# Kernel tuning notes

Measured on AMD Instinct MI355X. Metric: run time of the kernel, lower is better.

## Reference

```python
import jax, jax.numpy as jnp
import numpy as np

D_SAMPLE = 256
TEMPERATURE = 1.0
BETA = 0.5


def setup_inputs() -> dict:
    key = jax.random.key(0)
    k1, k2, k3, k4 = jax.random.split(key, 4)
    K, D = 64, 1_000_000
    client_tokens = jax.random.normal(k1, (K, D), dtype=jnp.float32)
    global_token = jax.random.normal(k2, (1, D), dtype=jnp.float32)
    # attention_net params: Linear(512,128) -> ReLU -> Linear(128,1)
    W1 = jax.random.normal(k3, (2 * D_SAMPLE, 128), dtype=jnp.float32) * (1.0 / np.sqrt(2 * D_SAMPLE))
    b1 = jnp.zeros((128,), dtype=jnp.float32)
    W2 = jax.random.normal(k4, (128, 1), dtype=jnp.float32) * (1.0 / np.sqrt(128))
    b2 = jnp.zeros((1,), dtype=jnp.float32)
    return {"client_tokens": client_tokens, "global_token": global_token,
            "W1": W1, "b1": b1, "W2": W2, "b2": b2}


def _fixed_size_sample(tokens):
    # gather d_input_sample columns with indices = arange(256) % L
    L = tokens.shape[1]
    idx = jnp.arange(D_SAMPLE, dtype=jnp.int32) % L
    return tokens[:, idx]  # [N, 256]


def reference(client_tokens, global_token, W1, b1, W2, b2):
    K, D = client_tokens.shape
    expanded_global = jnp.broadcast_to(global_token, (K, D))
    client_samples = _fixed_size_sample(client_tokens)      # [K, 256]
    global_samples = _fixed_size_sample(expanded_global)    # [K, 256]
    attn_in = jnp.concatenate([client_samples, global_samples], axis=1).astype(jnp.float32)  # [K, 512]
    h = jax.nn.relu(attn_in @ W1 + b1)                       # [K, 128]
    scores = h @ W2 + b2                                     # [K, 1]
    attention_weights = jax.nn.softmax(scores / TEMPERATURE, axis=0)  # [K, 1]
    fused_by_clients = jnp.sum(client_tokens * attention_weights, axis=0, keepdims=True)  # [1, D]
    fused_token = (1.0 - BETA) * global_token + BETA * fused_by_clients
    return fused_token
```

## Files before the change

kernel.cpp:

```cpp
#include <hip/hip_runtime.h>

#define D_SAMPLE 256
#define KCLIENTS 64
#define NH 128

__global__ void lf_scores_kernel(const float* __restrict__ client,
                                 const float* __restrict__ globalt,
                                 const float* __restrict__ W1,
                                 const float* __restrict__ b1,
                                 const float* __restrict__ W2,
                                 const float* __restrict__ b2,
                                 float* __restrict__ scores,
                                 int D) {
    const int k = blockIdx.x;
    const int t = threadIdx.x;

    __shared__ float attn[2 * D_SAMPLE];
    __shared__ float ph[4][NH];
    __shared__ float red[2];

    if (t < D_SAMPLE)       attn[t] = client[(size_t)k * D + t];
    else                    attn[t] = globalt[t - D_SAMPLE];
    __syncthreads();

    const int q = t >> 7;
    const int j = t & (NH - 1);
    const float* __restrict__ w1p = W1 + (size_t)(q * 128) * NH + j;
    const float* __restrict__ xp  = attn + q * 128;

    float acc = 0.0f;
#pragma unroll 8
    for (int i = 0; i < 128; ++i)
        acc = fmaf(xp[i], w1p[(size_t)i * NH], acc);
    ph[q][j] = acc;
    __syncthreads();

    if (t < NH) {
        float h = b1[j] + ph[0][j] + ph[1][j] + ph[2][j] + ph[3][j];
        h = fmaxf(h, 0.0f);
        float v = h * W2[j];
#pragma unroll
        for (int off = 32; off > 0; off >>= 1)
            v += __shfl_down(v, off, 64);
        if ((t & 63) == 0) red[t >> 6] = v;
    }
    __syncthreads();
    if (t == 0) scores[k] = red[0] + red[1] + b2[0];
}

__global__ void lf_fuse_kernel(const float* __restrict__ client,
                               const float* __restrict__ globalt,
                               const float* __restrict__ scores,
                               float* __restrict__ out,
                               int D4) {
    __shared__ float w[KCLIENTS];
    const int t = threadIdx.x;
    if (t < KCLIENTS) {
        float s = scores[t];
        float m = s;
#pragma unroll
        for (int off = 32; off > 0; off >>= 1)
            m = fmaxf(m, __shfl_xor(m, off, 64));
        float e = __expf(s - m);
        float sum = e;
#pragma unroll
        for (int off = 32; off > 0; off >>= 1)
            sum += __shfl_xor(sum, off, 64);
        w[t] = e / sum;
    }
    __syncthreads();

    const float4* __restrict__ c4 = (const float4*)client;
    const float4* __restrict__ g4 = (const float4*)globalt;
    float4* __restrict__ o4 = (float4*)out;

    int idx = blockIdx.x * blockDim.x + t;
    int stride = gridDim.x * blockDim.x;

    for (int d = idx; d < D4; d += stride) {
        float4 acc = make_float4(0.f, 0.f, 0.f, 0.f);
#pragma unroll 8
        for (int k = 0; k < KCLIENTS; ++k) {
            const float wk = w[k];
            const float4 c = c4[(size_t)k * D4 + d];
            acc.x = fmaf(wk, c.x, acc.x);
            acc.y = fmaf(wk, c.y, acc.y);
            acc.z = fmaf(wk, c.z, acc.z);
            acc.w = fmaf(wk, c.w, acc.w);
        }
        const float4 g = g4[d];
        float4 r;
        r.x = 0.5f * g.x + 0.5f * acc.x;
        r.y = 0.5f * g.y + 0.5f * acc.y;
        r.z = 0.5f * g.z + 0.5f * acc.z;
        r.w = 0.5f * g.w + 0.5f * acc.w;
        o4[d] = r;
    }
}

extern "C" void kernel_launch(void* const* d_in, const int* in_sizes, int n_in,
                              void* d_out, int out_size, void* d_ws, size_t ws_size,
                              hipStream_t stream) {
    const float* client  = (const float*)d_in[0];
    const float* globalt = (const float*)d_in[1];
    const float* W1      = (const float*)d_in[2];
    const float* b1      = (const float*)d_in[3];
    const float* W2      = (const float*)d_in[4];
    const float* b2      = (const float*)d_in[5];
    float* out = (float*)d_out;

    const int D = in_sizes[0] / KCLIENTS;
    const int D4 = D / 4;

    float* scores = (float*)d_ws;

    lf_scores_kernel<<<KCLIENTS, 512, 0, stream>>>(client, globalt, W1, b1, W2, b2,
                                                   scores, D);

    const int block = 256;
    int grid = (D4 + block - 1) / block;
    lf_fuse_kernel<<<grid, block, 0, stream>>>(client, globalt, scores, out, D4);
}
```

Before: 51.33 us.

## Fuse score and fusion kernels via cooperative launch with pre-sync prefetch

Merges the attention-score kernel and the weighted-sum kernel into one cooperative kernel. The first 64 blocks compute the per-client scores, then every block prefetches its first six client rows into shared memory before a grid-wide sync. After the sync, each block computes the softmax and accumulates the remaining rows from global memory. The aim is to remove the second kernel launch and hide the score computation behind useful loads. In exchange it adds a grid-wide barrier and about 24KB of shared memory per block, and it relies on all 977 blocks being co-resident, which the cooperative launch requires but whose return status is not checked.

```diff
diff --git a/kernel.cpp b/kernel.cpp
--- a/kernel.cpp
+++ b/kernel.cpp
@@ -1,60 +1,82 @@
 #include <hip/hip_runtime.h>
+#include <hip/hip_cooperative_groups.h>
+
+namespace cg = cooperative_groups;
 
 #define D_SAMPLE 256
 #define KCLIENTS 64
 #define NH 128
+#define STAGE_K 6
+#define BLOCK 256
 
-__global__ void lf_scores_kernel(const float* __restrict__ client,
-                                 const float* __restrict__ globalt,
-                                 const float* __restrict__ W1,
-                                 const float* __restrict__ b1,
-                                 const float* __restrict__ W2,
-                                 const float* __restrict__ b2,
-                                 float* __restrict__ scores,
-                                 int D) {
-    const int k = blockIdx.x;
+__global__ __launch_bounds__(BLOCK, 4)
+void lf_fused_kernel(const float* __restrict__ client,
+                     const float* __restrict__ globalt,
+                     const float* __restrict__ W1,
+                     const float* __restrict__ b1,
+                     const float* __restrict__ W2,
+                     const float* __restrict__ b2,
+                     float* __restrict__ scores,
+                     float* __restrict__ out,
+                     int D, int D4) {
+    __shared__ float4 stage[STAGE_K][BLOCK];
+    __shared__ float  w[KCLIENTS];
+    __shared__ float  ph[2][NH];
+    __shared__ float  red[2];
+    __shared__ float  attn[2 * D_SAMPLE];
+
     const int t = threadIdx.x;
+    const int b = blockIdx.x;
+    const float4* __restrict__ c4 = (const float4*)client;
+    const float4* __restrict__ g4 = (const float4*)globalt;
+    float4* __restrict__ o4 = (float4*)out;
 
-    __shared__ float attn[2 * D_SAMPLE];
-    __shared__ float ph[4][NH];
-    __shared__ float red[2];
+    const int d = b * BLOCK + t;
 
-    if (t < D_SAMPLE)       attn[t] = client[(size_t)k * D + t];
-    else                    attn[t] = globalt[t - D_SAMPLE];
-    __syncthreads();
+    if (b < KCLIENTS) {
+        const int k = b;
+        attn[t]            = client[(size_t)k * D + t];
+        attn[D_SAMPLE + t] = globalt[t];
+        __syncthreads();
 
-    const int q = t >> 7;
-    const int j = t & (NH - 1);
-    const float* __restrict__ w1p = W1 + (size_t)(q * 128) * NH + j;
-    const float* __restrict__ xp  = attn + q * 128;
+        const int q = t >> 7;
+        const int j = t & (NH - 1);
+        const float* __restrict__ w1p = W1 + (size_t)(q * D_SAMPLE) * NH + j;
+        const float* __restrict__ xp  = attn + q * D_SAMPLE;
 
-    float acc = 0.0f;
+        float acc = 0.0f;
 #pragma unroll 8
-    for (int i = 0; i < 128; ++i)
-        acc = fmaf(xp[i], w1p[(size_t)i * NH], acc);
-    ph[q][j] = acc;
-    __syncthreads();
+        for (int i = 0; i < D_SAMPLE; ++i)
+            acc = fmaf(xp[i], w1p[(size_t)i * NH], acc);
+        ph[q][j] = acc;
+        __syncthreads();
 
-    if (t < NH) {
-        float h = b1[j] + ph[0][j] + ph[1][j] + ph[2][j] + ph[3][j];
-        h = fmaxf(h, 0.0f);
-        float v = h * W2[j];
+        if (t < NH) {
+            float h = b1[j] + ph[0][j] + ph[1][j];
+            h = fmaxf(h, 0.0f);
+            float v = h * W2[j];
 #pragma unroll
-        for (int off = 32; off > 0; off >>= 1)
-            v += __shfl_down(v, off, 64);
-        if ((t & 63) == 0) red[t >> 6] = v;
+            for (int off = 32; off > 0; off >>= 1)
+                v += __shfl_down(v, off, 64);
+            if ((t & 63) == 0) red[t >> 6] = v;
+        }
+        __syncthreads();
+        if (t == 0) {
+            scores[k] = red[0] + red[1] + b2[0];
+            __threadfence();
+        }
+        __syncthreads();
     }
-    __syncthreads();
-    if (t == 0) scores[k] = red[0] + red[1] + b2[0];
-}
 
-__global__ void lf_fuse_kernel(const float* __restrict__ client,
-                               const float* __restrict__ globalt,
-                               const float* __restrict__ scores,
-                               float* __restrict__ out,
-                               int D4) {
-    __shared__ float w[KCLIENTS];
-    const int t = threadIdx.x;
+#pragma unroll
+    for (int k = 0; k < STAGE_K; ++k) {
+        float4 v = make_float4(0.f, 0.f, 0.f, 0.f);
+        if (d < D4) v = c4[(size_t)k * D4 + d];
+        stage[k][t] = v;
+    }
+
+    cg::this_grid().sync();
+
     if (t < KCLIENTS) {
         float s = scores[t];
         float m = s;
@@ -70,17 +92,19 @@
     }
     __syncthreads();
 
-    const float4* __restrict__ c4 = (const float4*)client;
-    const float4* __restrict__ g4 = (const float4*)globalt;
-    float4* __restrict__ o4 = (float4*)out;
-
-    int idx = blockIdx.x * blockDim.x + t;
-    int stride = gridDim.x * blockDim.x;
-
-    for (int d = idx; d < D4; d += stride) {
+    if (d < D4) {
         float4 acc = make_float4(0.f, 0.f, 0.f, 0.f);
-#pragma unroll 8
-        for (int k = 0; k < KCLIENTS; ++k) {
+#pragma unroll
+        for (int k = 0; k < STAGE_K; ++k) {
+            const float wk = w[k];
+            const float4 c = stage[k][t];
+            acc.x = fmaf(wk, c.x, acc.x);
+            acc.y = fmaf(wk, c.y, acc.y);
+            acc.z = fmaf(wk, c.z, acc.z);
+            acc.w = fmaf(wk, c.w, acc.w);
+        }
+#pragma unroll 4
+        for (int k = STAGE_K; k < KCLIENTS; ++k) {
             const float wk = w[k];
             const float4 c = c4[(size_t)k * D4 + d];
             acc.x = fmaf(wk, c.x, acc.x);
@@ -109,15 +133,19 @@
     const float* b2      = (const float*)d_in[5];
     float* out = (float*)d_out;
 
-    const int D = in_sizes[0] / KCLIENTS;
-    const int D4 = D / 4;
+    int D  = in_sizes[0] / KCLIENTS;
+    int D4 = D / 4;
 
     float* scores = (float*)d_ws;
 
-    lf_scores_kernel<<<KCLIENTS, 512, 0, stream>>>(client, globalt, W1, b1, W2, b2,
-                                                   scores, D);
+    int grid = (D4 + BLOCK - 1) / BLOCK;
 
-    const int block = 256;
-    int grid = (D4 + block - 1) / block;
-    lf_fuse_kernel<<<grid, block, 0, stream>>>(client, globalt, scores, out, D4);
+    void* args[] = {
+        (void*)&client, (void*)&globalt, (void*)&W1, (void*)&b1,
+        (void*)&W2, (void*)&b2, (void*)&scores, (void*)&out,
+        (void*)&D, (void*)&D4
+    };
+    hipLaunchCooperativeKernel((const void*)lf_fused_kernel,
+                               dim3(grid), dim3(BLOCK),
+                               args, 0, stream);
 }
```

After: 121.9 us. 137% more time.
